# Kernel tuning notes

Hardware: AMD Instinct MI355X
Metric: run time of the kernel (lower is better)

The kernel has to match this reference:

```python
import jax, jax.numpy as jnp
import numpy as np

D_MODEL = 1024
NUM_EXPERTS = 16
TOP_K = 2
TOP_C = 4  # min(M, max(4, 2*K))
RANK = 64  # max(4, d_model // 16) per choose_lowrank_r
TAU = 1.0


def setup_inputs() -> dict:
    key = jax.random.key(0)
    ks = jax.random.split(key, 7)
    B = 32768
    x = jax.random.normal(ks[0], (B, D_MODEL), dtype=jnp.float32)
    # shared encoder Linear(d, d) with bias
    We = jax.random.normal(ks[1], (D_MODEL, D_MODEL), dtype=jnp.float32) / np.sqrt(D_MODEL)
    be = jnp.zeros((D_MODEL,), dtype=jnp.float32)
    # gating Linear(d, M), no bias
    Wg = jax.random.normal(ks[2], (NUM_EXPERTS, D_MODEL), dtype=jnp.float32) / np.sqrt(D_MODEL)
    # per-expert LoRA weights: U: [M, r, d], V: [M, d, r], gamma: [M]
    U = jax.random.normal(ks[3], (NUM_EXPERTS, RANK, D_MODEL), dtype=jnp.float32) / np.sqrt(D_MODEL)
    V = jax.random.normal(ks[4], (NUM_EXPERTS, D_MODEL, RANK), dtype=jnp.float32) / np.sqrt(RANK)
    gamma = jnp.ones((NUM_EXPERTS,), dtype=jnp.float32)
    return {"x": x, "We": We, "be": be, "Wg": Wg, "U": U, "V": V, "gamma": gamma}


def reference(x, We, be, Wg, U, V, gamma):
    B = x.shape[0]
    encoded = x @ We.T + be                       # [B, d]
    logits = (encoded @ Wg.T) / TAU               # [B, M]
    # Top-C candidate selection, then Top-K among candidates
    topc_vals, topc_idx = jax.lax.top_k(logits, TOP_C)          # [B, C]
    topk_vals, pos_in_c = jax.lax.top_k(topc_vals, TOP_K)       # [B, K]
    topk_idx = jnp.take_along_axis(topc_idx, pos_in_c, axis=1)  # [B, K]
    # masked stable softmax over selected logits (matches _stable_masked_softmax)
    e = jnp.exp(topk_vals - jnp.max(topk_vals, axis=1, keepdims=True))
    w = e / (jnp.sum(e, axis=1, keepdims=True) + 1e-12)
    w = jnp.where(w > 1e-12, w, 0.0)  # keep_mask: drop negligible weights
    # scatter routing weights into dense [B, M] combine matrix
    w_full = jnp.zeros((B, NUM_EXPERTS), x.dtype).at[
        jnp.arange(B)[:, None], topk_idx].add(w)
    # expert residual delta: E(x) = x + gamma * V @ silu(U @ x)
    hidden = jax.nn.silu(jnp.einsum('bd,mrd->bmr', encoded, U))  # [B, M, r]
    delta = jnp.einsum('bmr,mdr,bm->bd', hidden, V, w_full * gamma[None, :])
    # y = encoded + sum_k w_k * (E_k(encoded) - encoded); sum_k w_k = 1
    return encoded + delta
```

## Files before the change

kernel.cpp:

```cpp
#include <hip/hip_runtime.h>
#include <stdint.h>

#define B_TOK 32768
#define DM 1024
#define NEXP 16
#define RK 64
#define NPAIR 256
#define TPT 64
#define HT 128
#define GRID_CMB 3072
#define GRID_HID 544
#define MAXTILE 1024

typedef unsigned short u16;
typedef __bf16 bf16x8 __attribute__((ext_vector_type(8)));
typedef float f32x4 __attribute__((ext_vector_type(4)));

__device__ __forceinline__ u16 f2bf(float f) {
  union { float f; uint32_t u; } v; v.f = f;
  return (u16)((v.u + 0x7fffu + ((v.u >> 16) & 1u)) >> 16);
}
__device__ __forceinline__ float bf2f(u16 u) {
  union { uint32_t i; float f; } v; v.i = ((uint32_t)u) << 16; return v.f;
}

__device__ __forceinline__ void gload_lds16(const void* g, void* l) {
  __builtin_amdgcn_global_load_lds(
      (const __attribute__((address_space(1))) void*)g,
      (__attribute__((address_space(3))) void*)l, 16, 0, 0);
}

__global__ void k_convert(const float* __restrict__ src, u16* __restrict__ dst, int n4) {
  int i = blockIdx.x * blockDim.x + threadIdx.x;
  int stride = gridDim.x * blockDim.x;
  for (; i < n4; i += stride) {
    float4 v = reinterpret_cast<const float4*>(src)[i];
    ushort4 o;
    o.x = f2bf(v.x); o.y = f2bf(v.y); o.z = f2bf(v.z); o.w = f2bf(v.w);
    reinterpret_cast<ushort4*>(dst)[i] = o;
  }
}

__global__ void k_wgeff(const float* __restrict__ Wg, const float* __restrict__ We,
                        const float* __restrict__ be,
                        float* __restrict__ Wgeff, float* __restrict__ gbias) {
  int e = blockIdx.y;
  int d = blockIdx.x * 256 + threadIdx.x;
  double acc = 0.0;
  for (int k = 0; k < DM; ++k)
    acc += (double)Wg[e * DM + k] * (double)We[k * DM + d];
  Wgeff[e * DM + d] = (float)acc;
  if (blockIdx.x == 0 && threadIdx.x == 0) {
    double s = 0.0;
    for (int k = 0; k < DM; ++k) s += (double)be[k] * (double)Wg[e * DM + k];
    gbias[e] = (float)s;
  }
}

#define GT 64
#define GD 128

__global__ __launch_bounds__(256) void k_gating(
    const float* __restrict__ x, u16* __restrict__ x_bf,
    const float* __restrict__ Wgeff, const float* __restrict__ gbias,
    const float* __restrict__ gamma,
    int* __restrict__ tk_pid, float* __restrict__ tk_w0, float* __restrict__ tk_w1,
    int* __restrict__ counts_p, int* __restrict__ counts_e) {
  __shared__ float xs[GT][GD + 4];
  __shared__ float wsd[NEXP][GD + 4];
  __shared__ float lg[GT][NEXP + 2];
  __shared__ int bcnt[NPAIR];
  __shared__ int bexp[NEXP];
  const int tid = threadIdx.x;
  const int tok0 = blockIdx.x * GT;
  const int t0 = (tid >> 3) * 2;
  const int e0 = (tid & 7) * 2;
  bcnt[tid] = 0;
  if (tid < NEXP) bexp[tid] = 0;

  double acc00 = 0.0, acc01 = 0.0, acc10 = 0.0, acc11 = 0.0;

  for (int c = 0; c < DM; c += GD) {
    __syncthreads();
    #pragma unroll
    for (int v = 0; v < (GT * GD / 4) / 256; ++v) {
      int idx = tid + v * 256;
      int r = idx >> 5, cc = idx & 31;
      float4 v4 = *reinterpret_cast<const float4*>(x + (size_t)(tok0 + r) * DM + c + cc * 4);
      *reinterpret_cast<float4*>(&xs[r][cc * 4]) = v4;
      ushort4 o;
      o.x = f2bf(v4.x); o.y = f2bf(v4.y); o.z = f2bf(v4.z); o.w = f2bf(v4.w);
      *reinterpret_cast<ushort4*>(x_bf + (size_t)(tok0 + r) * DM + c + cc * 4) = o;
    }
    #pragma unroll
    for (int v = 0; v < (NEXP * GD / 4) / 256; ++v) {
      int idx = tid + v * 256;
      int r = idx >> 5, cc = idx & 31;
      *reinterpret_cast<float4*>(&wsd[r][cc * 4]) =
          *reinterpret_cast<const float4*>(Wgeff + (size_t)r * DM + c + cc * 4);
    }
    __syncthreads();
    #pragma unroll 8
    for (int d = 0; d < GD; d += 4) {
      float4 xa = *reinterpret_cast<const float4*>(&xs[t0][d]);
      float4 xb = *reinterpret_cast<const float4*>(&xs[t0 + 1][d]);
      float4 wa = *reinterpret_cast<const float4*>(&wsd[e0][d]);
      float4 wb = *reinterpret_cast<const float4*>(&wsd[e0 + 1][d]);
      acc00 += (double)xa.x * wa.x + (double)xa.y * wa.y + (double)xa.z * wa.z + (double)xa.w * wa.w;
      acc01 += (double)xa.x * wb.x + (double)xa.y * wb.y + (double)xa.z * wb.z + (double)xa.w * wb.w;
      acc10 += (double)xb.x * wa.x + (double)xb.y * wa.y + (double)xb.z * wa.z + (double)xb.w * wa.w;
      acc11 += (double)xb.x * wb.x + (double)xb.y * wb.y + (double)xb.z * wb.z + (double)xb.w * wb.w;
    }
  }

  lg[t0][e0]         = (float)(acc00 + (double)gbias[e0]);
  lg[t0][e0 + 1]     = (float)(acc01 + (double)gbias[e0 + 1]);
  lg[t0 + 1][e0]     = (float)(acc10 + (double)gbias[e0]);
  lg[t0 + 1][e0 + 1] = (float)(acc11 + (double)gbias[e0 + 1]);
  __syncthreads();

  if (tid < GT) {
    int tok = tok0 + tid;
    float v0 = lg[tid][0]; int i0 = 0;
    #pragma unroll
    for (int j = 1; j < NEXP; ++j)
      if (lg[tid][j] > v0) { v0 = lg[tid][j]; i0 = j; }
    float v1 = -3.4e38f; int i1 = 0;
    #pragma unroll
    for (int j = 0; j < NEXP; ++j) {
      if (j == i0) continue;
      if (lg[tid][j] > v1) { v1 = lg[tid][j]; i1 = j; }
    }
    float e1 = expf(v1 - v0);
    float denom = 1.0f + e1 + 1e-12f;
    float w0 = 1.0f / denom, w1 = e1 / denom;
    if (!(w0 > 1e-12f)) w0 = 0.0f;
    if (!(w1 > 1e-12f)) w1 = 0.0f;
    int pid = i0 * 16 + i1;
    tk_pid[tok] = pid;
    tk_w0[tok] = w0 * gamma[i0];
    tk_w1[tok] = w1 * gamma[i1];
    atomicAdd(&bcnt[pid], 1);
    atomicAdd(&bexp[i0], 1);
    atomicAdd(&bexp[i1], 1);
  }
  __syncthreads();
  if (bcnt[tid] > 0) atomicAdd(&counts_p[tid], bcnt[tid]);
  if (tid < NEXP && bexp[tid] > 0) atomicAdd(&counts_e[tid], bexp[tid]);
}

__global__ __launch_bounds__(NPAIR) void k_scan(
    const int* __restrict__ counts_p, const int* __restrict__ counts_e,
    int* __restrict__ offs_p, int* __restrict__ curs_p,
    int* __restrict__ offs_e, int* __restrict__ curs_e,
    int* __restrict__ tp_pair, int* __restrict__ tp_loc, int* __restrict__ n_tp,
    int* __restrict__ th_exp, int* __restrict__ th_loc, int* __restrict__ n_th) {
  __shared__ int sc[NPAIR], st[NPAIR];
  __shared__ int seb[NEXP + 1], thb[NEXP + 1];
  const int tid = threadIdx.x;
  const int c = counts_p[tid];
  const int nt = (c + TPT - 1) / TPT;
  sc[tid] = c; st[tid] = nt;
  __syncthreads();
  for (int s = 1; s < NPAIR; s <<= 1) {
    int vc = 0, vt = 0;
    if (tid >= s) { vc = sc[tid - s]; vt = st[tid - s]; }
    __syncthreads();
    sc[tid] += vc; st[tid] += vt;
    __syncthreads();
  }
  const int offc = sc[tid] - c;
  const int offt = st[tid] - nt;
  offs_p[tid] = offc;
  curs_p[tid] = offc;
  if (tid == NPAIR - 1) { offs_p[NPAIR] = sc[tid]; n_tp[0] = st[tid]; }
  for (int q = 0; q < nt; ++q) { tp_pair[offt + q] = tid; tp_loc[offt + q] = q * TPT; }

  if (tid == 0) {
    int s = 0, s2 = 0;
    for (int e = 0; e < NEXP; ++e) {
      seb[e] = s; thb[e] = s2;
      int ce = counts_e[e];
      s += ce; s2 += (ce + HT - 1) / HT;
    }
    seb[NEXP] = s; thb[NEXP] = s2;
    n_th[0] = s2;
  }
  __syncthreads();
  if (tid <= NEXP) offs_e[tid] = seb[tid];
  if (tid < NEXP) {
    curs_e[tid] = seb[tid];
    int ce = counts_e[tid];
    int ntt = (ce + HT - 1) / HT;
    for (int q = 0; q < ntt; ++q) { th_exp[thb[tid] + q] = tid; th_loc[thb[tid] + q] = q * HT; }
  }
}

__global__ __launch_bounds__(256) void k_scatter(
    const int* __restrict__ tk_pid, const float* __restrict__ tk_w0,
    const float* __restrict__ tk_w1,
    int* __restrict__ curs_p, int* __restrict__ curs_e,
    int* __restrict__ a_tok, int* __restrict__ a_h0,
    int* __restrict__ a_h1,
    int* __restrict__ e_tok, float* __restrict__ e_w) {
  __shared__ int hp[NPAIR];
  __shared__ int he[NEXP];
  __shared__ int bp[NPAIR];
  __shared__ int beB[NEXP];
  const int tid = threadIdx.x;
  const int tok = blockIdx.x * 256 + tid;
  hp[tid] = 0;
  if (tid < NEXP) he[tid] = 0;
  __syncthreads();

  const int pid = tk_pid[tok];
  const int i0 = pid >> 4, i1 = pid & 15;
  const int rp = atomicAdd(&hp[pid], 1);
  const int r0 = atomicAdd(&he[i0], 1);
  const int r1 = atomicAdd(&he[i1], 1);
  __syncthreads();

  if (hp[tid] > 0) bp[tid] = atomicAdd(&curs_p[tid], hp[tid]);
  if (tid < NEXP && he[tid] > 0) beB[tid] = atomicAdd(&curs_e[tid], he[tid]);
  __syncthreads();

  const int posp = bp[pid] + rp;
  const int pos0 = beB[i0] + r0;
  const int pos1 = beB[i1] + r1;
  a_tok[posp] = tok;
  a_h0[posp] = pos0;
  a_h1[posp] = pos1;
  e_tok[pos0] = tok; e_w[pos0] = tk_w0[tok];
  e_tok[pos1] = tok; e_w[pos1] = tk_w1[tok];
}

__global__ __launch_bounds__(256) void k_encoder(
    const u16* __restrict__ A, const u16* __restrict__ Bm,
    const float* __restrict__ bias, u16* __restrict__ Cb) {
  __shared__ __align__(16) u16 As[128 * 32];
  __shared__ __align__(16) u16 Bs[128 * 32];
  const int nwg = gridDim.x * gridDim.y;
  const int orig = blockIdx.y * gridDim.x + blockIdx.x;
  const int qq = nwg >> 3;
  const int swz = (orig & 7) * qq + (orig >> 3);
  const int m0 = (swz / gridDim.x) * 128, n0 = (swz % gridDim.x) * 128;
  const int tid = threadIdx.x;
  const int lane = tid & 63, wave = tid >> 6;
  const int wr = wave >> 1, wc = wave & 1;

  f32x4 acc[4][4];
  #pragma unroll
  for (int i = 0; i < 4; ++i)
    #pragma unroll
    for (int j = 0; j < 4; ++j) acc[i][j] = (f32x4){0.f, 0.f, 0.f, 0.f};

  const int srow = tid >> 2;
  const int scol = (((tid & 3) ^ (srow & 3)) * 8);
  const int lrow = lane & 15;
  const int lk = (((lane >> 4) ^ (lrow & 3)) * 8);

  const u16* ga1 = A + (size_t)(m0 + srow) * DM + scol;
  const u16* ga2 = A + (size_t)(m0 + 64 + srow) * DM + scol;
  const u16* gb1 = Bm + (size_t)(n0 + srow) * DM + scol;
  const u16* gb2 = Bm + (size_t)(n0 + 64 + srow) * DM + scol;

  for (int k0 = 0; k0 < DM; k0 += 32) {
    __syncthreads();
    gload_lds16(ga1 + k0, As + tid * 8);
    gload_lds16(ga2 + k0, As + 2048 + tid * 8);
    gload_lds16(gb1 + k0, Bs + tid * 8);
    gload_lds16(gb2 + k0, Bs + 2048 + tid * 8);
    __syncthreads();
    bf16x8 a[4], b[4];
    #pragma unroll
    for (int mi = 0; mi < 4; ++mi)
      a[mi] = *reinterpret_cast<const bf16x8*>(&As[(wr * 64 + mi * 16 + lrow) * 32 + lk]);
    #pragma unroll
    for (int nj = 0; nj < 4; ++nj)
      b[nj] = *reinterpret_cast<const bf16x8*>(&Bs[(wc * 64 + nj * 16 + lrow) * 32 + lk]);
    #pragma unroll
    for (int mi = 0; mi < 4; ++mi)
      #pragma unroll
      for (int nj = 0; nj < 4; ++nj)
        acc[mi][nj] = __builtin_amdgcn_mfma_f32_16x16x32_bf16(a[mi], b[nj], acc[mi][nj], 0, 0, 0);
  }

  const int orow = (lane >> 4) * 4, ocol = lane & 15;
  #pragma unroll
  for (int mi = 0; mi < 4; ++mi) {
    #pragma unroll
    for (int nj = 0; nj < 4; ++nj) {
      int gcol = n0 + wc * 64 + nj * 16 + ocol;
      float bv = bias[gcol];
      #pragma unroll
      for (int r = 0; r < 4; ++r) {
        int grow = m0 + wr * 64 + mi * 16 + orow + r;
        Cb[(size_t)grow * DM + gcol] = f2bf(acc[mi][nj][r] + bv);
      }
    }
  }
}

__global__ __launch_bounds__(256) void k_hidden(
    const u16* __restrict__ Enc, const u16* __restrict__ Ub,
    const int* __restrict__ offs_e, const int* __restrict__ th_exp,
    const int* __restrict__ th_loc, const int* __restrict__ n_th,
    const int* __restrict__ e_tok, const float* __restrict__ e_w,
    u16* __restrict__ Hws) {
  const int bswz = (blockIdx.x & 7) * (GRID_HID >> 3) + (blockIdx.x >> 3);
  if (bswz >= n_th[0]) return;
  const int e = th_exp[bswz];
  const int loc0 = th_loc[bswz];
  const int base = offs_e[e];
  const int cnt = offs_e[e + 1] - base;
  const int tid = threadIdx.x;
  const int lane = tid & 63, wave = tid >> 6;
  const int lrow = lane & 15;
  const int lkb = (lane >> 4) * 16;

  __shared__ float s_ew[HT];
  __shared__ __align__(16) u16 Us[64 * 512];
  if (tid < HT) {
    int i = loc0 + tid;
    s_ew[tid] = (i < cnt) ? e_w[base + i] : 0.0f;
  }

  const u16* aP[2];
  #pragma unroll
  for (int mi = 0; mi < 2; ++mi) {
    int ridx = loc0 + wave * 32 + mi * 16 + lrow;
    int v = ridx < cnt;
    int tok = e_tok[base + (v ? ridx : 0)];
    aP[mi] = Enc + (size_t)tok * DM + (lane >> 4) * 8;
  }

  f32x4 acc[2][4];
  #pragma unroll
  for (int i = 0; i < 2; ++i)
    #pragma unroll
    for (int j = 0; j < 4; ++j) acc[i][j] = (f32x4){0.f, 0.f, 0.f, 0.f};

  const char* Ue = (const char*)(Ub + (size_t)e * RK * DM);

  for (int half = 0; half < 2; ++half) {
    __syncthreads();
    #pragma unroll
    for (int it = 0; it < 16; ++it) {
      int D = (tid + it * 256) * 16;
      int row = D >> 10, bo = D & 1023;
      int sbo = bo ^ ((row & 7) << 4);
      gload_lds16(Ue + (size_t)row * 2048 + half * 1024 + sbo, ((char*)Us) + D);
    }
    __syncthreads();
    #pragma unroll 4
    for (int step = 0; step < 16; ++step) {
      const int k0 = half * 512 + step * 32;
      bf16x8 b[4];
      #pragma unroll
      for (int nj = 0; nj < 4; ++nj) {
        int n = nj * 16 + lrow;
        int bofs = n * 1024 + ((step * 64 + lkb) ^ ((n & 7) << 4));
        b[nj] = *reinterpret_cast<const bf16x8*>(((const char*)Us) + bofs);
      }
      bf16x8 a0 = *reinterpret_cast<const bf16x8*>(aP[0] + k0);
      bf16x8 a1 = *reinterpret_cast<const bf16x8*>(aP[1] + k0);
      #pragma unroll
      for (int nj = 0; nj < 4; ++nj) {
        acc[0][nj] = __builtin_amdgcn_mfma_f32_16x16x32_bf16(a0, b[nj], acc[0][nj], 0, 0, 0);
        acc[1][nj] = __builtin_amdgcn_mfma_f32_16x16x32_bf16(a1, b[nj], acc[1][nj], 0, 0, 0);
      }
    }
  }

  #pragma unroll
  for (int mi = 0; mi < 2; ++mi)
    #pragma unroll
    for (int nj = 0; nj < 4; ++nj)
      #pragma unroll
      for (int rr = 0; rr < 4; ++rr) {
        int rloc = wave * 32 + mi * 16 + (lane >> 4) * 4 + rr;
        if (loc0 + rloc < cnt) {
          float z = acc[mi][nj][rr];
          float h = z / (1.0f + expf(-z)) * s_ew[rloc];
          Hws[(size_t)(base + loc0 + rloc) * RK + nj * 16 + (lane & 15)] = f2bf(h);
        }
      }
}

__global__ __launch_bounds__(256) void k_combine(
    const u16* __restrict__ Enc, const u16* __restrict__ Vb,
    const u16* __restrict__ Hws, const int* __restrict__ offs_p,
    const int* __restrict__ tp_pair, const int* __restrict__ tp_loc,
    const int* __restrict__ n_tp, const int* __restrict__ a_tok,
    const int* __restrict__ a_h0, const int* __restrict__ a_h1,
    float* __restrict__ Out) {
  const int bswz = (blockIdx.x & 7) * (GRID_CMB >> 3) + (blockIdx.x >> 3);
  const int t = bswz >> 2;
  const int p = bswz & 3;
  if (t >= n_tp[0]) return;
  const int pid = tp_pair[t];
  const int pe0 = pid >> 4, pe1 = pid & 15;
  const int base = offs_p[pid];
  const int cnt = offs_p[pid + 1] - base;
  const int loc0 = tp_loc[t];
  const int tid = threadIdx.x;
  const int lane = tid & 63, wave = tid >> 6;

  __shared__ int s_tok[TPT];
  __shared__ int s_h0[TPT];
  __shared__ int s_h1[TPT];
  __shared__ int s_val[TPT];
  if (tid < TPT) {
    int idx = loc0 + tid;
    int v = idx < cnt;
    int pp = base + (v ? idx : 0);
    s_val[tid] = v;
    s_tok[tid] = a_tok[pp];
    s_h0[tid] = a_h0[pp];
    s_h1[tid] = a_h1[pp];
  }
  __syncthreads();

  const int lrow = lane & 15, lk = (lane >> 4) * 8;
  const int col0 = p * 256 + wave * 64;

  bf16x8 hb[4][4];
  #pragma unroll
  for (int kk = 0; kk < 4; ++kk)
    #pragma unroll
    for (int tf = 0; tf < 4; ++tf) {
      int tok = tf * 16 + lrow;
      int hidx = (kk < 2) ? s_h0[tok] : s_h1[tok];
      hb[kk][tf] = *reinterpret_cast<const bf16x8*>(
          Hws + (size_t)hidx * RK + (kk & 1) * 32 + lk);
    }

  ushort4 encv[4][4];
  #pragma unroll
  for (int mi = 0; mi < 4; ++mi)
    #pragma unroll
    for (int tf = 0; tf < 4; ++tf) {
      int tok = tf * 16 + (lane & 15);
      int d = col0 + mi * 16 + (lane >> 4) * 4;
      encv[mi][tf] = *reinterpret_cast<const ushort4*>(Enc + (size_t)s_tok[tok] * DM + d);
    }

  const u16* V0 = Vb + (size_t)pe0 * DM * RK;
  const u16* V1 = Vb + (size_t)pe1 * DM * RK;

  f32x4 acc2[4][4];
  #pragma unroll
  for (int i = 0; i < 4; ++i)
    #pragma unroll
    for (int j = 0; j < 4; ++j) acc2[i][j] = (f32x4){0.f, 0.f, 0.f, 0.f};

  #pragma unroll
  for (int kk = 0; kk < 4; ++kk) {
    const u16* Vsel = (kk < 2) ? V0 : V1;
    const int kof = (kk & 1) * 32 + lk;
    #pragma unroll
    for (int mi = 0; mi < 4; ++mi) {
      int d = col0 + mi * 16 + lrow;
      bf16x8 va = *reinterpret_cast<const bf16x8*>(Vsel + (size_t)d * RK + kof);
      #pragma unroll
      for (int tf = 0; tf < 4; ++tf)
        acc2[mi][tf] = __builtin_amdgcn_mfma_f32_16x16x32_bf16(va, hb[kk][tf], acc2[mi][tf], 0, 0, 0);
    }
  }

  #pragma unroll
  for (int mi = 0; mi < 4; ++mi)
    #pragma unroll
    for (int tf = 0; tf < 4; ++tf) {
      int tok = tf * 16 + (lane & 15);
      if (!s_val[tok]) continue;
      int d = col0 + mi * 16 + (lane >> 4) * 4;
      size_t ro = (size_t)s_tok[tok] * DM + d;
      ushort4 ev = encv[mi][tf];
      float4 o;
      o.x = acc2[mi][tf][0] + bf2f(ev.x);
      o.y = acc2[mi][tf][1] + bf2f(ev.y);
      o.z = acc2[mi][tf][2] + bf2f(ev.z);
      o.w = acc2[mi][tf][3] + bf2f(ev.w);
      *reinterpret_cast<float4*>(Out + ro) = o;
    }
}

extern "C" void kernel_launch(void* const* d_in, const int* in_sizes, int n_in,
                              void* d_out, int out_size, void* d_ws, size_t ws_size,
                              hipStream_t stream) {
  const float* x = (const float*)d_in[0];
  const float* We = (const float*)d_in[1];
  const float* be = (const float*)d_in[2];
  const float* Wg = (const float*)d_in[3];
  const float* U = (const float*)d_in[4];
  const float* V = (const float*)d_in[5];
  const float* gamma = (const float*)d_in[6];
  float* Out = (float*)d_out;

  char* ws = (char*)d_ws;
  size_t off = 0;
  auto alloc = [&](size_t bytes) -> void* {
    void* p = ws + off;
    off += (bytes + 255) & ~(size_t)255;
    return p;
  };
  u16* x_bf   = (u16*)alloc((size_t)B_TOK * DM * 2);
  u16* enc_bf = (u16*)alloc((size_t)B_TOK * DM * 2);
  u16* We_bf  = (u16*)alloc((size_t)DM * DM * 2);
  u16* U_bf   = (u16*)alloc((size_t)NEXP * RK * DM * 2);
  u16* V_bf   = (u16*)alloc((size_t)NEXP * DM * RK * 2);
  u16* Hws    = (u16*)alloc(((size_t)2 * B_TOK + HT) * RK * 2);
  float* Wgeff = (float*)alloc((size_t)NEXP * DM * 4);
  float* gbias = (float*)alloc(NEXP * 4);
  int* tk_pid  = (int*)alloc((size_t)B_TOK * 4);
  float* tk_w0 = (float*)alloc((size_t)B_TOK * 4);
  float* tk_w1 = (float*)alloc((size_t)B_TOK * 4);
  int* counts_p = (int*)alloc(NPAIR * 4);
  int* counts_e = (int*)alloc(NEXP * 4);
  int* offs_p   = (int*)alloc((NPAIR + 1) * 4);
  int* curs_p   = (int*)alloc(NPAIR * 4);
  int* offs_e   = (int*)alloc((NEXP + 1) * 4);
  int* curs_e   = (int*)alloc(NEXP * 4);
  int* tp_pair  = (int*)alloc(MAXTILE * 4);
  int* tp_loc   = (int*)alloc(MAXTILE * 4);
  int* n_tp     = (int*)alloc(256);
  int* th_exp   = (int*)alloc(MAXTILE * 4);
  int* th_loc   = (int*)alloc(MAXTILE * 4);
  int* n_th     = (int*)alloc(256);
  int* a_tok   = (int*)alloc((size_t)B_TOK * 4);
  int* a_h0    = (int*)alloc((size_t)B_TOK * 4);
  int* a_h1    = (int*)alloc((size_t)B_TOK * 4);
  int* e_tok   = (int*)alloc(((size_t)2 * B_TOK + HT) * 4);
  float* e_w   = (float*)alloc(((size_t)2 * B_TOK + HT) * 4);
  (void)ws_size; (void)in_sizes; (void)n_in; (void)out_size;

  hipMemsetAsync(counts_p, 0, NPAIR * 4, stream);
  hipMemsetAsync(counts_e, 0, NEXP * 4, stream);

  k_convert<<<256, 256, 0, stream>>>(We, We_bf, DM * DM / 4);
  k_convert<<<256, 256, 0, stream>>>(U, U_bf, NEXP * RK * DM / 4);
  k_convert<<<256, 256, 0, stream>>>(V, V_bf, NEXP * DM * RK / 4);
  k_wgeff<<<dim3(4, 16), 256, 0, stream>>>(Wg, We, be, Wgeff, gbias);
  k_gating<<<B_TOK / GT, 256, 0, stream>>>(x, x_bf, Wgeff, gbias, gamma,
                                           tk_pid, tk_w0, tk_w1, counts_p, counts_e);
  k_scan<<<1, NPAIR, 0, stream>>>(counts_p, counts_e, offs_p, curs_p, offs_e, curs_e,
                                  tp_pair, tp_loc, n_tp, th_exp, th_loc, n_th);
  k_scatter<<<B_TOK / 256, 256, 0, stream>>>(tk_pid, tk_w0, tk_w1, curs_p, curs_e,
                                             a_tok, a_h0, a_h1, e_tok, e_w);
  k_encoder<<<dim3(DM / 128, B_TOK / 128), 256, 0, stream>>>(x_bf, We_bf, be, enc_bf);
  k_hidden<<<GRID_HID, 256, 0, stream>>>(enc_bf, U_bf, offs_e, th_exp, th_loc, n_th,
                                         e_tok, e_w, Hws);
  k_combine<<<GRID_CMB, 256, 0, stream>>>(enc_bf, V_bf, Hws, offs_p, tp_pair, tp_loc,
                                          n_tp, a_tok, a_h0, a_h1, Out);
}
```

Baseline: 378.8 us.

## Double-buffer encoder GEMM LDS tiles and prefetch next K-slice

The encoder GEMM now keeps two LDS buffers per operand and issues the global-to-LDS loads for the next K-slice before computing on the current one. It waits with an explicit vmcnt so those loads overlap the MFMA work, instead of syncing twice per iteration with nothing in flight. The XOR swizzle on LDS columns is also dropped, which simplifies addressing but may bring back LDS bank conflicts on the fragment reads. LDS use doubles, which could lower occupancy.

```diff
diff --git a/kernel.cpp b/kernel.cpp
--- a/kernel.cpp
+++ b/kernel.cpp
@@ -237,8 +237,8 @@
 __global__ __launch_bounds__(256) void k_encoder(
     const u16* __restrict__ A, const u16* __restrict__ Bm,
     const float* __restrict__ bias, u16* __restrict__ Cb) {
-  __shared__ __align__(16) u16 As[128 * 32];
-  __shared__ __align__(16) u16 Bs[128 * 32];
+  __shared__ __align__(16) u16 As[2 * 128 * 32];
+  __shared__ __align__(16) u16 Bs[2 * 128 * 32];
   const int nwg = gridDim.x * gridDim.y;
   const int orig = blockIdx.y * gridDim.x + blockIdx.x;
   const int qq = nwg >> 3;
@@ -255,29 +255,58 @@
     for (int j = 0; j < 4; ++j) acc[i][j] = (f32x4){0.f, 0.f, 0.f, 0.f};
 
   const int srow = tid >> 2;
-  const int scol = (((tid & 3) ^ (srow & 3)) * 8);
-  const int lrow = lane & 15;
-  const int lk = (((lane >> 4) ^ (lrow & 3)) * 8);
+  const int scol = (tid & 3) * 8;
+  const int lrow = lane & 15, lk = (lane >> 4) * 8;
+  const int ldst = srow * 32 + scol;
 
   const u16* ga1 = A + (size_t)(m0 + srow) * DM + scol;
   const u16* ga2 = A + (size_t)(m0 + 64 + srow) * DM + scol;
   const u16* gb1 = Bm + (size_t)(n0 + srow) * DM + scol;
   const u16* gb2 = Bm + (size_t)(n0 + 64 + srow) * DM + scol;
 
-  for (int k0 = 0; k0 < DM; k0 += 32) {
-    __syncthreads();
-    gload_lds16(ga1 + k0, As + tid * 8);
-    gload_lds16(ga2 + k0, As + 2048 + tid * 8);
-    gload_lds16(gb1 + k0, Bs + tid * 8);
-    gload_lds16(gb2 + k0, Bs + 2048 + tid * 8);
-    __syncthreads();
+  gload_lds16(ga1, As + ldst);
+  gload_lds16(ga2, As + 2048 + ldst);
+  gload_lds16(gb1, Bs + ldst);
+  gload_lds16(gb2, Bs + 2048 + ldst);
+
+  for (int t = 0; t < 31; ++t) {
+    const int cur = t & 1;
+    const int nxt = cur ^ 1;
+    const int k1 = (t + 1) * 32;
+    gload_lds16(ga1 + k1, As + nxt * 4096 + ldst);
+    gload_lds16(ga2 + k1, As + nxt * 4096 + 2048 + ldst);
+    gload_lds16(gb1 + k1, Bs + nxt * 4096 + ldst);
+    gload_lds16(gb2 + k1, Bs + nxt * 4096 + 2048 + ldst);
+    asm volatile("s_waitcnt vmcnt(4)" ::: "memory");
+    __builtin_amdgcn_s_barrier();
+    const u16* Ar = As + cur * 4096;
+    const u16* Br = Bs + cur * 4096;
     bf16x8 a[4], b[4];
     #pragma unroll
     for (int mi = 0; mi < 4; ++mi)
-      a[mi] = *reinterpret_cast<const bf16x8*>(&As[(wr * 64 + mi * 16 + lrow) * 32 + lk]);
+      a[mi] = *reinterpret_cast<const bf16x8*>(&Ar[(wr * 64 + mi * 16 + lrow) * 32 + lk]);
     #pragma unroll
     for (int nj = 0; nj < 4; ++nj)
-      b[nj] = *reinterpret_cast<const bf16x8*>(&Bs[(wc * 64 + nj * 16 + lrow) * 32 + lk]);
+      b[nj] = *reinterpret_cast<const bf16x8*>(&Br[(wc * 64 + nj * 16 + lrow) * 32 + lk]);
+    #pragma unroll
+    for (int mi = 0; mi < 4; ++mi)
+      #pragma unroll
+      for (int nj = 0; nj < 4; ++nj)
+        acc[mi][nj] = __builtin_amdgcn_mfma_f32_16x16x32_bf16(a[mi], b[nj], acc[mi][nj], 0, 0, 0);
+    __builtin_amdgcn_s_barrier();
+  }
+  asm volatile("s_waitcnt vmcnt(0)" ::: "memory");
+  __builtin_amdgcn_s_barrier();
+  {
+    const u16* Ar = As + 4096;
+    const u16* Br = Bs + 4096;
+    bf16x8 a[4], b[4];
+    #pragma unroll
+    for (int mi = 0; mi < 4; ++mi)
+      a[mi] = *reinterpret_cast<const bf16x8*>(&Ar[(wr * 64 + mi * 16 + lrow) * 32 + lk]);
+    #pragma unroll
+    for (int nj = 0; nj < 4; ++nj)
+      b[nj] = *reinterpret_cast<const bf16x8*>(&Br[(wc * 64 + nj * 16 + lrow) * 32 + lk]);
     #pragma unroll
     for (int mi = 0; mi < 4; ++mi)
       #pragma unroll
```

Result: slower. 392.4 us (+3.6%).

## Double encoder GEMM K-tile to 64 and merge weight conversions into one launch

Applied to the files above, without the earlier changes.

The encoder GEMM now stages 64-wide K slices per iteration instead of 32, using an 8-way XOR swizzle and two MFMA sub-steps per slice. This halves the number of barrier pairs and loop iterations over K. Separately, the three fp32-to-bf16 weight conversions are merged into one kernel launch that picks its segment from the block index, removing two launches. The larger LDS tile doubles shared memory per block, which may lower occupancy.

```diff
diff --git a/kernel.cpp b/kernel.cpp
--- a/kernel.cpp
+++ b/kernel.cpp
@@ -30,14 +30,21 @@
       (__attribute__((address_space(3))) void*)l, 16, 0, 0);
 }
 
-__global__ void k_convert(const float* __restrict__ src, u16* __restrict__ dst, int n4) {
-  int i = blockIdx.x * blockDim.x + threadIdx.x;
-  int stride = gridDim.x * blockDim.x;
-  for (; i < n4; i += stride) {
-    float4 v = reinterpret_cast<const float4*>(src)[i];
+__global__ void k_convert3(const float* __restrict__ s0, u16* __restrict__ d0,
+                           const float* __restrict__ s1, u16* __restrict__ d1,
+                           const float* __restrict__ s2, u16* __restrict__ d2) {
+  const int seg = blockIdx.x >> 8;
+  const int bid = blockIdx.x & 255;
+  const float* src = (seg == 0) ? s0 : (seg == 1) ? s1 : s2;
+  u16* dst = (seg == 0) ? d0 : (seg == 1) ? d1 : d2;
+  int i = bid * 256 + threadIdx.x;
+  #pragma unroll
+  for (int v = 0; v < 4; ++v) {
+    int idx = i + v * 65536;
+    float4 f = reinterpret_cast<const float4*>(src)[idx];
     ushort4 o;
-    o.x = f2bf(v.x); o.y = f2bf(v.y); o.z = f2bf(v.z); o.w = f2bf(v.w);
-    reinterpret_cast<ushort4*>(dst)[i] = o;
+    o.x = f2bf(f.x); o.y = f2bf(f.y); o.z = f2bf(f.z); o.w = f2bf(f.w);
+    reinterpret_cast<ushort4*>(dst)[idx] = o;
   }
 }
 
@@ -237,8 +244,8 @@
 __global__ __launch_bounds__(256) void k_encoder(
     const u16* __restrict__ A, const u16* __restrict__ Bm,
     const float* __restrict__ bias, u16* __restrict__ Cb) {
-  __shared__ __align__(16) u16 As[128 * 32];
-  __shared__ __align__(16) u16 Bs[128 * 32];
+  __shared__ __align__(16) u16 As[128 * 64];
+  __shared__ __align__(16) u16 Bs[128 * 64];
   const int nwg = gridDim.x * gridDim.y;
   const int orig = blockIdx.y * gridDim.x + blockIdx.x;
   const int qq = nwg >> 3;
@@ -247,6 +254,7 @@
   const int tid = threadIdx.x;
   const int lane = tid & 63, wave = tid >> 6;
   const int wr = wave >> 1, wc = wave & 1;
+  const int lrow = lane & 15, lhi = lane >> 4;
 
   f32x4 acc[4][4];
   #pragma unroll
@@ -254,38 +262,54 @@
     #pragma unroll
     for (int j = 0; j < 4; ++j) acc[i][j] = (f32x4){0.f, 0.f, 0.f, 0.f};
 
-  const int srow = tid >> 2;
-  const int scol = (((tid & 3) ^ (srow & 3)) * 8);
-  const int lrow = lane & 15;
-  const int lk = (((lane >> 4) ^ (lrow & 3)) * 8);
-
-  const u16* ga1 = A + (size_t)(m0 + srow) * DM + scol;
-  const u16* ga2 = A + (size_t)(m0 + 64 + srow) * DM + scol;
-  const u16* gb1 = Bm + (size_t)(n0 + srow) * DM + scol;
-  const u16* gb2 = Bm + (size_t)(n0 + 64 + srow) * DM + scol;
-
-  for (int k0 = 0; k0 < DM; k0 += 32) {
-    __syncthreads();
-    gload_lds16(ga1 + k0, As + tid * 8);
-    gload_lds16(ga2 + k0, As + 2048 + tid * 8);
-    gload_lds16(gb1 + k0, Bs + tid * 8);
-    gload_lds16(gb2 + k0, Bs + 2048 + tid * 8);
-    __syncthreads();
-    bf16x8 a[4], b[4];
-    #pragma unroll
-    for (int mi = 0; mi < 4; ++mi)
-      a[mi] = *reinterpret_cast<const bf16x8*>(&As[(wr * 64 + mi * 16 + lrow) * 32 + lk]);
-    #pragma unroll
-    for (int nj = 0; nj < 4; ++nj)
-      b[nj] = *reinterpret_cast<const bf16x8*>(&Bs[(wc * 64 + nj * 16 + lrow) * 32 + lk]);
-    #pragma unroll
-    for (int mi = 0; mi < 4; ++mi)
+  const u16* gA0; const u16* gA1; const u16* gA2; const u16* gA3;
+  const u16* gB0; const u16* gB1; const u16* gB2; const u16* gB3;
+  int dOf0, dOf1, dOf2, dOf3;
+  {
+    int slot, row, c, sc;
+    slot = tid;         row = slot >> 3; c = slot & 7; sc = (c ^ (row & 7)) * 8;
+    gA0 = A + (size_t)(m0 + row) * DM + sc; gB0 = Bm + (size_t)(n0 + row) * DM + sc; dOf0 = slot * 8;
+    slot = tid + 256;   row = slot >> 3; c = slot & 7; sc = (c ^ (row & 7)) * 8;
+    gA1 = A + (size_t)(m0 + row) * DM + sc; gB1 = Bm + (size_t)(n0 + row) * DM + sc; dOf1 = slot * 8;
+    slot = tid + 512;   row = slot >> 3; c = slot & 7; sc = (c ^ (row & 7)) * 8;
+    gA2 = A + (size_t)(m0 + row) * DM + sc; gB2 = Bm + (size_t)(n0 + row) * DM + sc; dOf2 = slot * 8;
+    slot = tid + 768;   row = slot >> 3; c = slot & 7; sc = (c ^ (row & 7)) * 8;
+    gA3 = A + (size_t)(m0 + row) * DM + sc; gB3 = Bm + (size_t)(n0 + row) * DM + sc; dOf3 = slot * 8;
+  }
+
+  const int rk0 = ((0 + lhi) ^ (lrow & 7)) * 8;
+  const int rk1 = ((4 + lhi) ^ (lrow & 7)) * 8;
+
+  for (int k0 = 0; k0 < DM; k0 += 64) {
+    __syncthreads();
+    gload_lds16(gA0 + k0, As + dOf0);
+    gload_lds16(gA1 + k0, As + dOf1);
+    gload_lds16(gA2 + k0, As + dOf2);
+    gload_lds16(gA3 + k0, As + dOf3);
+    gload_lds16(gB0 + k0, Bs + dOf0);
+    gload_lds16(gB1 + k0, Bs + dOf1);
+    gload_lds16(gB2 + k0, Bs + dOf2);
+    gload_lds16(gB3 + k0, Bs + dOf3);
+    __syncthreads();
+    #pragma unroll
+    for (int kk = 0; kk < 2; ++kk) {
+      const int rk = kk ? rk1 : rk0;
+      bf16x8 a[4], b[4];
+      #pragma unroll
+      for (int mi = 0; mi < 4; ++mi)
+        a[mi] = *reinterpret_cast<const bf16x8*>(&As[(wr * 64 + mi * 16 + lrow) * 64 + rk]);
       #pragma unroll
       for (int nj = 0; nj < 4; ++nj)
-        acc[mi][nj] = __builtin_amdgcn_mfma_f32_16x16x32_bf16(a[mi], b[nj], acc[mi][nj], 0, 0, 0);
-  }
-
-  const int orow = (lane >> 4) * 4, ocol = lane & 15;
+        b[nj] = *reinterpret_cast<const bf16x8*>(&Bs[(wc * 64 + nj * 16 + lrow) * 64 + rk]);
+      #pragma unroll
+      for (int mi = 0; mi < 4; ++mi)
+        #pragma unroll
+        for (int nj = 0; nj < 4; ++nj)
+          acc[mi][nj] = __builtin_amdgcn_mfma_f32_16x16x32_bf16(a[mi], b[nj], acc[mi][nj], 0, 0, 0);
+    }
+  }
+
+  const int orow = lhi * 4, ocol = lrow;
   #pragma unroll
   for (int mi = 0; mi < 4; ++mi) {
     #pragma unroll
@@ -538,9 +562,7 @@
   hipMemsetAsync(counts_p, 0, NPAIR * 4, stream);
   hipMemsetAsync(counts_e, 0, NEXP * 4, stream);
 
-  k_convert<<<256, 256, 0, stream>>>(We, We_bf, DM * DM / 4);
-  k_convert<<<256, 256, 0, stream>>>(U, U_bf, NEXP * RK * DM / 4);
-  k_convert<<<256, 256, 0, stream>>>(V, V_bf, NEXP * DM * RK / 4);
+  k_convert3<<<768, 256, 0, stream>>>(We, We_bf, U, U_bf, V, V_bf);
   k_wgeff<<<dim3(4, 16), 256, 0, stream>>>(Wg, We, be, Wgeff, gbias);
   k_gating<<<B_TOK / GT, 256, 0, stream>>>(x, x_bf, Wgeff, gbias, gamma,
                                            tk_pid, tk_w0, tk_w1, counts_p, counts_e);
```

After: 366.4 us. -3.3%, faster.
